# Kernel tuning notes

Measured on AMD Instinct MI355X. Metric: run time of the kernel, lower is better.

Reference implementation:

```python
import jax, jax.numpy as jnp
import numpy as np

T = 48  # top-T from init

def setup_inputs() -> dict:
    key = jax.random.key(0)
    ks = jax.random.split(key, 8)
    B, C, H, W = 16, 512, 32, 32
    tc = C // 8
    return {
        "x": jax.random.normal(ks[0], (B, C, H, W), jnp.float32),
        "fW": jax.random.normal(ks[1], (tc, C), jnp.float32) * 0.05,
        "fb": jax.random.normal(ks[2], (tc,), jnp.float32) * 0.05,
        "gW": jax.random.normal(ks[3], (tc, C), jnp.float32) * 0.05,
        "gb": jax.random.normal(ks[4], (tc,), jnp.float32) * 0.05,
        "hW": jax.random.normal(ks[5], (C, C), jnp.float32) * 0.05,
        "hb": jax.random.normal(ks[6], (C,), jnp.float32) * 0.05,
        "scale": jax.random.normal(ks[7], (1,), jnp.float32),
    }

def reference(x, fW, fb, gW, gb, hW, hb, scale):
    B, C, H, W = x.shape
    tc = fW.shape[0]
    HW = H * W
    # normalize by Frobenius norm over (batch, channel) -> [H, W]
    xn = x / jnp.linalg.norm(x, axis=(0, 1))[None, None]  # [B,C,H,W]
    # 1x1 convs, output already channel-last [B,H,W,out]
    f = jnp.einsum('bchw,oc->bhwo', xn, fW) + fb          # [B,H,W,tc]
    g = jnp.einsum('bchw,oc->bhwo', xn, gW) + gb          # [B,H,W,tc]
    h = jnp.einsum('bchw,oc->bhwo', xn, hW) + hb          # [B,H,W,C]
    xp = jnp.transpose(xn, (0, 2, 3, 1))                  # [B,H,W,C]
    # scores: queries H-major, keys W-major (faithful to permute(0,3,2,1).reshape)
    g_keys = jnp.transpose(g, (0, 3, 2, 1)).reshape(B, tc, HW)  # [B,tc,W*H]
    s = jnp.matmul(f.reshape(B, HW, tc), g_keys)          # [B,HW,HW]
    beta = jax.nn.softmax(s, axis=-1)
    o = jnp.matmul(beta, h.reshape(B, HW, C)).reshape(B, H, W, C)
    fdd = scale * o + xp                                  # [B,H,W,C]
    # per-batch correlation: fdd[b] ([H,W,C]) @ fdd[b].reshape(C,HW)
    corr = jnp.einsum('bhwc,bcn->bhwn', fdd, fdd.reshape(B, C, HW))  # [B,H,W,HW]
    top = jax.lax.top_k(corr, T)[0]                       # descending top-T values
    top = jax.nn.relu(top)
    top = top / jnp.linalg.norm(top, axis=(0, 1))[None, None]  # norm over (B,H) -> [W,T]
    return jnp.transpose(top, (0, 3, 1, 2))               # [B,T,H,W]
```

## Files before the change

kernel.cpp:

```cpp
#include <hip/hip_runtime.h>
#include <cstdint>
#include <cstddef>

#define B_   16
#define C_   512
#define H_   32
#define W_   32
#define HW_  1024
#define TC_  64
#define T_   48

typedef unsigned short u16;
typedef __attribute__((ext_vector_type(8))) short short8v;
typedef __attribute__((ext_vector_type(4))) float f32x4;

__device__ __forceinline__ u16 tobf(float x) {
    unsigned u = __float_as_uint(x);
    return (u16)((u + 0x7FFFu + ((u >> 16) & 1u)) >> 16);
}
__device__ __forceinline__ float frombf(u16 h) {
    return __uint_as_float(((unsigned)h) << 16);
}

__device__ __forceinline__ void gld16(const void* g, void* l) {
    __builtin_amdgcn_global_load_lds(
        (const __attribute__((address_space(1))) void*)g,
        (__attribute__((address_space(3))) void*)l, 16, 0, 0);
}

__global__ void k_colsq(const float* __restrict__ x, float* __restrict__ partial) {
    int bid = blockIdx.x;
    int col = (bid & 3) * 256 + threadIdx.x;
    int r0  = (bid >> 2) * 256;
    const float* p = x + (size_t)r0 * HW_ + col;
    float s = 0.f;
    for (int r = 0; r < 256; ++r) { float v = p[(size_t)r * HW_]; s += v * v; }
    partial[(size_t)(bid >> 2) * HW_ + col] = s;
}

__global__ void k_rsqrt(const float* __restrict__ partial, float* __restrict__ ninv) {
    int i = blockIdx.x * 256 + threadIdx.x;
    if (i < HW_) {
        float s = 0.f;
        for (int r = 0; r < 32; ++r) s += partial[(size_t)r * HW_ + i];
        ninv[i] = rsqrtf(s);
    }
}

__global__ void k_transpose(const float* __restrict__ x, const float* __restrict__ ninv,
                            u16* __restrict__ obH) {
    __shared__ float tile[32][33];
    int b  = blockIdx.z;
    int m0 = blockIdx.x * 32, c0 = blockIdx.y * 32;
    int tx = threadIdx.x, ty = threadIdx.y;
    const float* xb = x + (size_t)b * C_ * HW_;
    #pragma unroll
    for (int j = 0; j < 32; j += 8)
        tile[ty + j][tx] = xb[(size_t)(c0 + ty + j) * HW_ + m0 + tx];
    __syncthreads();
    size_t base = (size_t)b * HW_ * C_;
    #pragma unroll
    for (int j = 0; j < 32; j += 8) {
        int m = m0 + ty + j;
        obH[base + (size_t)m * C_ + c0 + tx] = tobf(tile[tx][ty + j] * ninv[m]);
    }
}

__global__ void k_packW(const float* __restrict__ in, u16* __restrict__ oh) {
    size_t i = (size_t)blockIdx.x * 256 + threadIdx.x;
    oh[i] = tobf(in[i]);
}
__global__ void k_packFG(const float* __restrict__ fW, const float* __restrict__ gW,
                         const float* __restrict__ fb, const float* __restrict__ gb,
                         u16* __restrict__ oh, float* __restrict__ fgb) {
    int idx = blockIdx.x * 256 + threadIdx.x;
    int row = idx >> 9, c = idx & 511;
    float v = (row < 64) ? fW[row * 512 + c] : gW[(row - 64) * 512 + c];
    oh[idx] = tobf(v);
    if (idx < 128) fgb[idx] = (idx < 64) ? fb[idx] : gb[idx - 64];
}

template<int PERMB, int EPI>
__global__ __launch_bounds__(256) void k_gemm1(
    const u16* __restrict__ A, const u16* __restrict__ Bm,
    const float* __restrict__ bias,
    float* __restrict__ Cf, u16* __restrict__ Ch,
    const float* __restrict__ scaleP,
    int N, int K, int lda, int ldb, long sA, long sB, long sC)
{
    __shared__ u16 lds[2 * 8192];
    const int b = blockIdx.z;
    const u16* pA = A + (size_t)b * sA;
    const u16* pB = Bm + (size_t)b * sB;
    const int m0 = blockIdx.y * 128, n0 = blockIdx.x * 128;
    const int tid = threadIdx.x, wave = tid >> 6, lane = tid & 63;
    const int wm = wave >> 1, wn = wave & 1;
    const int g = lane >> 4;

    f32x4 acc[4][4];
    #pragma unroll
    for (int i = 0; i < 4; ++i)
        #pragma unroll
        for (int j = 0; j < 4; ++j) { f32x4 z = {0.f,0.f,0.f,0.f}; acc[i][j] = z; }

    auto STAGE = [&](int kt, int half) {
        const int k0 = kt << 5;
        u16* lb = lds + half * 8192;
        #pragma unroll
        for (int q = 0; q < 4; ++q) {
            int ci = wave * 4 + q;
            bool isA = ci < 8;
            int li = ci & 7;
            const u16* gp = isA ? pA : pB;
            int ld = isA ? lda : ldb;
            int rb = isA ? m0 : n0;
            int rp = li * 8 + (lane >> 3);
            int gg = (lane & 7) ^ (rp & 7);
            int r  = rp * 2 + (gg >> 2);
            int kc = k0 + (gg & 3) * 8;
            int rowg = rb + r;
            if (PERMB && !isA) rowg = ((rowg & 31) << 5) | (rowg >> 5);
            gld16(gp + (size_t)rowg * ld + kc,
                  lb + (isA ? 0 : 4096) + li * 512 + lane * 8);
        }
    };
    auto COMPUTE = [&](int half) {
        const u16* As = lds + half * 8192;
        const u16* Bs = As + 4096;
        short8v av[4];
        #pragma unroll
        for (int i = 0; i < 4; ++i) {
            int r = wm * 64 + i * 16 + (lane & 15);
            int rp = r >> 1, gg = ((r & 1) << 2) + g;
            av[i] = *(const short8v*)(As + rp * 64 + ((gg ^ (rp & 7)) << 3));
        }
        #pragma unroll
        for (int j = 0; j < 4; ++j) {
            int r = wn * 64 + j * 16 + (lane & 15);
            int rp = r >> 1, gg = ((r & 1) << 2) + g;
            short8v bv = *(const short8v*)(Bs + rp * 64 + ((gg ^ (rp & 7)) << 3));
            #pragma unroll
            for (int i = 0; i < 4; ++i)
                acc[i][j] = __builtin_amdgcn_mfma_f32_16x16x32_bf16(av[i], bv, acc[i][j], 0, 0, 0);
        }
    };

    const int nkt = K >> 5;
    STAGE(0, 0);
    int cur = 0;
    for (int kt = 0; kt < nkt; ++kt) {
        if (kt + 1 < nkt) {
            STAGE(kt + 1, cur ^ 1);
            asm volatile("s_waitcnt vmcnt(4)" ::: "memory");
        } else {
            asm volatile("s_waitcnt vmcnt(0)" ::: "memory");
        }
        __builtin_amdgcn_s_barrier();
        __builtin_amdgcn_sched_barrier(0);
        COMPUTE(cur);
        __builtin_amdgcn_sched_barrier(0);
        __builtin_amdgcn_s_barrier();
        cur ^= 1;
    }

    const float sc = (EPI == 2) ? scaleP[0] : 0.f;
    const int colbase = n0 + wn * 64 + (lane & 15);
    const int rowbase = m0 + wm * 64 + ((lane >> 4) << 2);
    #pragma unroll
    for (int i = 0; i < 4; ++i)
        #pragma unroll
        for (int j = 0; j < 4; ++j) {
            int col = colbase + j * 16;
            #pragma unroll
            for (int rg = 0; rg < 4; ++rg) {
                int row = rowbase + i * 16 + rg;
                size_t idx = (size_t)b * sC + (size_t)row * N + col;
                float a = acc[i][j][rg];
                if (EPI == 0)      Cf[idx] = a;
                else if (EPI == 2) Ch[idx] = tobf(sc * a + frombf(Ch[idx]));
                else if (EPI == 4) Ch[idx] = tobf(a);
                else if (EPI == 5) Ch[idx] = tobf(a + bias[row]);
                else               Ch[idx] = tobf(a + bias[col]);
            }
        }
}

template<int PERMB, int EPI>
__global__ __launch_bounds__(512) void k_gemm2(
    const u16* __restrict__ A, const u16* __restrict__ Bm,
    const float* __restrict__ bias,
    float* __restrict__ Cf, u16* __restrict__ Ch,
    const float* __restrict__ scaleP,
    int N, int K, int lda, int ldb, long sA, long sB, long sC)
{
    __shared__ u16 lds[2 * 12288];
    const int b = blockIdx.z;
    const u16* pA = A + (size_t)b * sA;
    const u16* pB = Bm + (size_t)b * sB;
    const int m0 = blockIdx.y * 128, n0 = blockIdx.x * 256;
    const int tid = threadIdx.x, wave = tid >> 6, lane = tid & 63;
    const int wm = wave >> 2, wn = wave & 3;
    const int g = lane >> 4;

    f32x4 acc[4][4];
    #pragma unroll
    for (int i = 0; i < 4; ++i)
        #pragma unroll
        for (int j = 0; j < 4; ++j) { f32x4 z = {0.f,0.f,0.f,0.f}; acc[i][j] = z; }

    auto STAGE = [&](int kt, int half) {
        const int k0 = kt << 5;
        u16* lb = lds + half * 12288;
        #pragma unroll
        for (int q = 0; q < 3; ++q) {
            int ci = wave * 3 + q;
            bool isA = ci < 8;
            int li = isA ? ci : ci - 8;
            const u16* gp = isA ? pA : pB;
            int ld = isA ? lda : ldb;
            int rb = isA ? m0 : n0;
            int rp = li * 8 + (lane >> 3);
            int gg = (lane & 7) ^ (rp & 7);
            int r  = rp * 2 + (gg >> 2);
            int kc = k0 + (gg & 3) * 8;
            int rowg = rb + r;
            if (PERMB && !isA) rowg = ((rowg & 31) << 5) | (rowg >> 5);
            gld16(gp + (size_t)rowg * ld + kc,
                  lb + (isA ? 0 : 4096) + li * 512 + lane * 8);
        }
    };
    auto COMPUTE = [&](int half) {
        const u16* As = lds + half * 12288;
        const u16* Bs = As + 4096;
        short8v av[4];
        #pragma unroll
        for (int i = 0; i < 4; ++i) {
            int r = wm * 64 + i * 16 + (lane & 15);
            int rp = r >> 1, gg = ((r & 1) << 2) + g;
            av[i] = *(const short8v*)(As + rp * 64 + ((gg ^ (rp & 7)) << 3));
        }
        #pragma unroll
        for (int j = 0; j < 4; ++j) {
            int r = wn * 64 + j * 16 + (lane & 15);
            int rp = r >> 1, gg = ((r & 1) << 2) + g;
            short8v bv = *(const short8v*)(Bs + rp * 64 + ((gg ^ (rp & 7)) << 3));
            #pragma unroll
            for (int i = 0; i < 4; ++i)
                acc[i][j] = __builtin_amdgcn_mfma_f32_16x16x32_bf16(av[i], bv, acc[i][j], 0, 0, 0);
        }
    };

    const int nkt = K >> 5;
    STAGE(0, 0);
    int cur = 0;
    for (int kt = 0; kt < nkt; ++kt) {
        if (kt + 1 < nkt) {
            STAGE(kt + 1, cur ^ 1);
            asm volatile("s_waitcnt vmcnt(3)" ::: "memory");
        } else {
            asm volatile("s_waitcnt vmcnt(0)" ::: "memory");
        }
        __builtin_amdgcn_s_barrier();
        __builtin_amdgcn_sched_barrier(0);
        COMPUTE(cur);
        __builtin_amdgcn_sched_barrier(0);
        __builtin_amdgcn_s_barrier();
        cur ^= 1;
    }

    const float sc = (EPI == 2) ? scaleP[0] : 0.f;
    const int colbase = n0 + wn * 64 + (lane & 15);
    const int rowbase = m0 + wm * 64 + ((lane >> 4) << 2);
    #pragma unroll
    for (int i = 0; i < 4; ++i)
        #pragma unroll
        for (int j = 0; j < 4; ++j) {
            int col = colbase + j * 16;
            #pragma unroll
            for (int rg = 0; rg < 4; ++rg) {
                int row = rowbase + i * 16 + rg;
                size_t idx = (size_t)b * sC + (size_t)row * N + col;
                float a = acc[i][j][rg];
                if (EPI == 0)      Cf[idx] = a;
                else if (EPI == 2) Ch[idx] = tobf(sc * a + frombf(Ch[idx]));
                else if (EPI == 4) Ch[idx] = tobf(a);
                else if (EPI == 5) Ch[idx] = tobf(a + bias[row]);
                else               Ch[idx] = tobf(a + bias[col]);
            }
        }
}

__global__ __launch_bounds__(256) void k_softmax(u16* __restrict__ S) {
    size_t row = blockIdx.x;
    u16* r = S + row * (size_t)HW_;
    int t = threadIdx.x;
    ushort4 raw = ((const ushort4*)r)[t];
    float v0 = frombf(raw.x), v1 = frombf(raw.y), v2 = frombf(raw.z), v3 = frombf(raw.w);

    __shared__ float redm[4], reds[4];
    int wid = t >> 6, lane = t & 63;

    float m = fmaxf(fmaxf(v0, v1), fmaxf(v2, v3));
    for (int o = 32; o > 0; o >>= 1) m = fmaxf(m, __shfl_down(m, o));
    if (lane == 0) redm[wid] = m;
    __syncthreads();
    if (t == 0) redm[0] = fmaxf(fmaxf(redm[0], redm[1]), fmaxf(redm[2], redm[3]));
    __syncthreads();
    m = redm[0];

    v0 = expf(v0 - m); v1 = expf(v1 - m); v2 = expf(v2 - m); v3 = expf(v3 - m);
    float s = v0 + v1 + v2 + v3;
    for (int o = 32; o > 0; o >>= 1) s += __shfl_down(s, o);
    if (lane == 0) reds[wid] = s;
    __syncthreads();
    if (t == 0) reds[0] = reds[0] + reds[1] + reds[2] + reds[3];
    __syncthreads();
    float inv = 1.f / reds[0];
    ushort4 o4;
    o4.x = tobf(v0 * inv); o4.y = tobf(v1 * inv);
    o4.z = tobf(v2 * inv); o4.w = tobf(v3 * inv);
    ((ushort4*)r)[t] = o4;
}

__global__ void k_tposeU1(const u16* __restrict__ src, u16* __restrict__ dst) {
    __shared__ u16 tile[32][33];
    int b = blockIdx.z;
    const u16* sb = src + (size_t)b * (C_ * HW_);
    u16* db = dst + (size_t)b * (C_ * HW_);
    int c0 = blockIdx.x * 32, r0 = blockIdx.y * 32;
    int tx = threadIdx.x, ty = threadIdx.y;
    #pragma unroll
    for (int j = 0; j < 32; j += 8)
        tile[ty + j][tx] = sb[(size_t)(r0 + ty + j) * HW_ + c0 + tx];
    __syncthreads();
    #pragma unroll
    for (int j = 0; j < 32; j += 8)
        db[(size_t)(c0 + ty + j) * C_ + r0 + tx] = tile[tx][ty + j];
}

__device__ __forceinline__ float sort64_desc(float v, int lane) {
    #pragma unroll
    for (int k = 2; k <= 64; k <<= 1) {
        #pragma unroll
        for (int j = k >> 1; j > 0; j >>= 1) {
            float o = __shfl_xor(v, j);
            bool takeMax = (((lane & k) == 0) == ((lane & j) == 0));
            v = takeMax ? fmaxf(v, o) : fminf(v, o);
        }
    }
    return v;
}
__device__ __forceinline__ float bmerge64_desc(float a, float b, int lane) {
    float br = __shfl(b, 63 - lane);
    float c = fmaxf(a, br);
    #pragma unroll
    for (int j = 32; j > 0; j >>= 1) {
        float o = __shfl_xor(c, j);
        c = ((lane & j) == 0) ? fmaxf(c, o) : fminf(c, o);
    }
    return c;
}

__global__ __launch_bounds__(256) void k_topk(const float* __restrict__ corr,
                                              float* __restrict__ topv) {
    __shared__ float buf[4][1024];
    int wave = threadIdx.x >> 6, lane = threadIdx.x & 63;
    int row = blockIdx.x * 4 + wave;
    const float4* rp = (const float4*)(corr + (size_t)row * HW_);

    float4 e[4];
    #pragma unroll
    for (int q = 0; q < 4; ++q) e[q] = rp[lane * 4 + q];

    float gm = -INFINITY;
    #pragma unroll
    for (int q = 0; q < 4; ++q)
        gm = fmaxf(gm, fmaxf(fmaxf(e[q].x, e[q].y), fmaxf(e[q].z, e[q].w)));
    float sorted = sort64_desc(gm, lane);
    float tau = __shfl(sorted, T_ - 1);

    int c = 0;
    #pragma unroll
    for (int q = 0; q < 4; ++q)
        c += (e[q].x >= tau) + (e[q].y >= tau) + (e[q].z >= tau) + (e[q].w >= tau);
    int sc = c;
    #pragma unroll
    for (int o = 1; o < 64; o <<= 1) {
        int t2 = __shfl_up(sc, o);
        if (lane >= o) sc += t2;
    }
    int off = sc - c;
    int cnt = __shfl(sc, 63);

    float* wb = buf[wave];
    #pragma unroll
    for (int q = 0; q < 4; ++q) {
        if (e[q].x >= tau) wb[off++] = e[q].x;
        if (e[q].y >= tau) wb[off++] = e[q].y;
        if (e[q].z >= tau) wb[off++] = e[q].z;
        if (e[q].w >= tau) wb[off++] = e[q].w;
    }

    float* orow = topv + (size_t)row * T_;
    if (cnt <= 64) {
        float a = (lane < cnt) ? wb[lane] : -INFINITY;
        a = sort64_desc(a, lane);
        if (lane < T_) orow[lane] = fmaxf(a, 0.f);
    } else if (cnt <= 128) {
        float a  = sort64_desc(wb[lane], lane);
        float b2 = sort64_desc((lane < cnt - 64) ? wb[64 + lane] : -INFINITY, lane);
        float m2 = bmerge64_desc(a, b2, lane);
        if (lane < T_) orow[lane] = fmaxf(m2, 0.f);
    } else {
        int P = 256; while (P < cnt) P <<= 1;
        for (int i = cnt + lane; i < P; i += 64) wb[i] = -INFINITY;
        for (int k = 2; k <= P; k <<= 1)
            for (int j = k >> 1; j > 0; j >>= 1)
                for (int t2 = lane; t2 < P; t2 += 64) {
                    int ixj = t2 ^ j;
                    if (ixj > t2) {
                        float a = wb[t2], b3 = wb[ixj];
                        bool desc = ((t2 & k) == 0);
                        if (desc ? (a < b3) : (a > b3)) { wb[t2] = b3; wb[ixj] = a; }
                    }
                }
        if (lane < T_) orow[lane] = fmaxf(wb[lane], 0.f);
    }
}

__global__ void k_colss(const float* __restrict__ topv, float* __restrict__ colss) {
    int o = blockIdx.x;
    int w = o / T_, t = o % T_;
    int lane = threadIdx.x;
    float s = 0.f;
    for (int i = lane; i < 512; i += 64) {
        int b = i >> 5, h = i & 31;
        float v = topv[(size_t)((b << 10) + (h << 5) + w) * T_ + t];
        s += v * v;
    }
    for (int off = 32; off > 0; off >>= 1) s += __shfl_down(s, off);
    if (lane == 0) colss[o] = s;
}

__global__ void k_final(const float* __restrict__ topv, const float* __restrict__ colss,
                        float* __restrict__ out) {
    int idx = blockIdx.x * 256 + threadIdx.x;
    if (idx >= B_ * T_ * HW_) return;
    int w = idx & 31;
    int h = (idx >> 5) & 31;
    int t = (idx >> 10) % T_;
    int b = idx / (T_ * HW_);
    float v = topv[(size_t)((b << 10) + (h << 5) + w) * T_ + t];
    out[idx] = v * rsqrtf(colss[w * T_ + t]);
}

extern "C" void kernel_launch(void* const* d_in, const int* in_sizes, int n_in,
                              void* d_out, int out_size, void* d_ws, size_t ws_size,
                              hipStream_t stream) {
    const float* x     = (const float*)d_in[0];
    const float* fW    = (const float*)d_in[1];
    const float* fb    = (const float*)d_in[2];
    const float* gW    = (const float*)d_in[3];
    const float* gb    = (const float*)d_in[4];
    const float* hW    = (const float*)d_in[5];
    const float* hb    = (const float*)d_in[6];
    const float* scale = (const float*)d_in[7];
    float* out = (float*)d_out;

    char* wsb = (char*)d_ws;
    float* part = (float*)(wsb + 0);
    float* ninv = (float*)(wsb + 131072);
    u16*   hWh  = (u16*)(wsb + 135168);
    u16*   fgWh = (u16*)(wsb + 1183744);
    float* fgb  = (float*)(wsb + 1445888);
    u16*   xnH  = (u16*)(wsb + 1446400);
    u16*   fgH  = (u16*)(wsb + 35000832);
    u16*   fgL  = (u16*)(wsb + 39195136);
    u16*   hvTH = (u16*)(wsb + 43389440);
    float* S    = (float*)(wsb + 76943872);
    float* topv = (float*)fgH;
    float* colss= (float*)fgL;
    u16*   Sp   = (u16*)S;

    const long sXn = 524288;
    const long sFG = 131072;
    const long sS  = 1048576;

    k_colsq<<<128, 256, 0, stream>>>(x, part);
    k_rsqrt<<<4, 256, 0, stream>>>(part, ninv);

    k_transpose<<<dim3(32, 16, 16), dim3(32, 8), 0, stream>>>(x, ninv, xnH);

    k_packW<<<1024, 256, 0, stream>>>(hW, hWh);
    k_packFG<<<256, 256, 0, stream>>>(fW, gW, fb, gb, fgWh, fgb);

    k_gemm1<0, 6><<<dim3(1, 8, 16), 256, 0, stream>>>(
        xnH, fgWh, fgb, nullptr, fgH, nullptr,
        128, 512, 512, 512, sXn, 0, sFG);

    k_gemm2<0, 5><<<dim3(4, 4, 16), 512, 0, stream>>>(
        hWh, xnH, hb, nullptr, hvTH, nullptr,
        1024, 512, 512, 512, 0, sXn, sXn);

    k_gemm2<1, 4><<<dim3(4, 8, 16), 512, 0, stream>>>(
        fgH, fgH + 64, nullptr, nullptr, Sp, nullptr,
        1024, 64, 128, 128, sFG, sFG, sS);

    k_softmax<<<B_ * HW_, 256, 0, stream>>>(Sp);

    k_gemm2<0, 2><<<dim3(2, 8, 16), 512, 0, stream>>>(
        Sp, hvTH, nullptr, nullptr, xnH, scale,
        512, 1024, 1024, 1024, sS, sXn, sXn);

    k_tposeU1<<<dim3(32, 16, 16), dim3(32, 8), 0, stream>>>(xnH, hvTH);

    k_gemm2<0, 0><<<dim3(4, 8, 16), 512, 0, stream>>>(
        xnH, hvTH, nullptr, S, nullptr, nullptr,
        1024, 512, 512, 512, sXn, sXn, sS);

    k_topk<<<B_ * HW_ / 4, 256, 0, stream>>>(S, topv);

    k_colss<<<W_ * T_, 64, 0, stream>>>(topv, colss);
    k_final<<<(B_ * T_ * HW_ + 255) / 256, 256, 0, stream>>>(topv, colss, out);
}
```

Before: 213.8 us.

## Fuse correlation GEMM with top-k selection and retile other GEMMs

Replaces the separate correlation GEMM and top-k kernels with one fused kernel. Each block computes a 32x1024 strip of the correlation matrix with bf16 MFMA, double-buffers its LDS loads, then selects the top-48 per row straight from LDS. This removes the write and re-read of the 64 MB fp32 score matrix. It also doubles the column-norm partial blocks and moves two GEMMs to the smaller-tile gemm1 variant with more blocks, and shrinks the workspace offsets to match. The fused kernel uses about 132 KB of LDS, which limits occupancy to one block per CU. Its grid is only 512 blocks.

```diff
diff --git a/kernel.cpp b/kernel.cpp
--- a/kernel.cpp
+++ b/kernel.cpp
@@ -31,10 +31,10 @@
 __global__ void k_colsq(const float* __restrict__ x, float* __restrict__ partial) {
     int bid = blockIdx.x;
     int col = (bid & 3) * 256 + threadIdx.x;
-    int r0  = (bid >> 2) * 256;
+    int r0  = (bid >> 2) * 128;
     const float* p = x + (size_t)r0 * HW_ + col;
     float s = 0.f;
-    for (int r = 0; r < 256; ++r) { float v = p[(size_t)r * HW_]; s += v * v; }
+    for (int r = 0; r < 128; ++r) { float v = p[(size_t)r * HW_]; s += v * v; }
     partial[(size_t)(bid >> 2) * HW_ + col] = s;
 }
 
@@ -42,7 +42,7 @@
     int i = blockIdx.x * 256 + threadIdx.x;
     if (i < HW_) {
         float s = 0.f;
-        for (int r = 0; r < 32; ++r) s += partial[(size_t)r * HW_ + i];
+        for (int r = 0; r < 64; ++r) s += partial[(size_t)r * HW_ + i];
         ninv[i] = rsqrtf(s);
     }
 }
@@ -361,70 +361,147 @@
     return c;
 }
 
-__global__ __launch_bounds__(256) void k_topk(const float* __restrict__ corr,
-                                              float* __restrict__ topv) {
-    __shared__ float buf[4][1024];
-    int wave = threadIdx.x >> 6, lane = threadIdx.x & 63;
-    int row = blockIdx.x * 4 + wave;
-    const float4* rp = (const float4*)(corr + (size_t)row * HW_);
-
-    float4 e[4];
-    #pragma unroll
-    for (int q = 0; q < 4; ++q) e[q] = rp[lane * 4 + q];
-
-    float gm = -INFINITY;
-    #pragma unroll
-    for (int q = 0; q < 4; ++q)
-        gm = fmaxf(gm, fmaxf(fmaxf(e[q].x, e[q].y), fmaxf(e[q].z, e[q].w)));
-    float sorted = sort64_desc(gm, lane);
-    float tau = __shfl(sorted, T_ - 1);
-
-    int c = 0;
-    #pragma unroll
-    for (int q = 0; q < 4; ++q)
-        c += (e[q].x >= tau) + (e[q].y >= tau) + (e[q].z >= tau) + (e[q].w >= tau);
-    int sc = c;
-    #pragma unroll
-    for (int o = 1; o < 64; o <<= 1) {
-        int t2 = __shfl_up(sc, o);
-        if (lane >= o) sc += t2;
-    }
-    int off = sc - c;
-    int cnt = __shfl(sc, 63);
-
-    float* wb = buf[wave];
-    #pragma unroll
-    for (int q = 0; q < 4; ++q) {
-        if (e[q].x >= tau) wb[off++] = e[q].x;
-        if (e[q].y >= tau) wb[off++] = e[q].y;
-        if (e[q].z >= tau) wb[off++] = e[q].z;
-        if (e[q].w >= tau) wb[off++] = e[q].w;
-    }
-
-    float* orow = topv + (size_t)row * T_;
-    if (cnt <= 64) {
-        float a = (lane < cnt) ? wb[lane] : -INFINITY;
-        a = sort64_desc(a, lane);
-        if (lane < T_) orow[lane] = fmaxf(a, 0.f);
-    } else if (cnt <= 128) {
-        float a  = sort64_desc(wb[lane], lane);
-        float b2 = sort64_desc((lane < cnt - 64) ? wb[64 + lane] : -INFINITY, lane);
-        float m2 = bmerge64_desc(a, b2, lane);
-        if (lane < T_) orow[lane] = fmaxf(m2, 0.f);
-    } else {
-        int P = 256; while (P < cnt) P <<= 1;
-        for (int i = cnt + lane; i < P; i += 64) wb[i] = -INFINITY;
-        for (int k = 2; k <= P; k <<= 1)
-            for (int j = k >> 1; j > 0; j >>= 1)
-                for (int t2 = lane; t2 < P; t2 += 64) {
-                    int ixj = t2 ^ j;
-                    if (ixj > t2) {
-                        float a = wb[t2], b3 = wb[ixj];
-                        bool desc = ((t2 & k) == 0);
-                        if (desc ? (a < b3) : (a > b3)) { wb[t2] = b3; wb[ixj] = a; }
-                    }
-                }
-        if (lane < T_) orow[lane] = fmaxf(wb[lane], 0.f);
+__global__ __launch_bounds__(512) void k_corrtopk(
+    const u16* __restrict__ A,
+    const u16* __restrict__ Bm,
+    float* __restrict__ topv)
+{
+    __shared__ u16 lds[67584];
+    const int b = blockIdx.y;
+    const int m0 = blockIdx.x * 32;
+    const u16* pA = A + (size_t)b * 524288;
+    const u16* pB = Bm + (size_t)b * 524288;
+    const int tid = threadIdx.x, wave = tid >> 6, lane = tid & 63;
+    const int g = lane >> 4;
+
+    f32x4 acc[2][8];
+    #pragma unroll
+    for (int i = 0; i < 2; ++i)
+        #pragma unroll
+        for (int j = 0; j < 8; ++j) { f32x4 z = {0.f,0.f,0.f,0.f}; acc[i][j] = z; }
+
+    auto STAGE = [&](int kt, int half) {
+        const int k0 = kt << 5;
+        u16* lb = lds + half * 33792;
+        #pragma unroll
+        for (int q = 0; q < 8; ++q) {
+            int li = wave * 8 + q;
+            int rp = li * 8 + (lane >> 3);
+            int gg = (lane & 7) ^ (rp & 7);
+            int r  = rp * 2 + (gg >> 2);
+            int kc = k0 + (gg & 3) * 8;
+            gld16(pB + (size_t)r * 512 + kc, lb + li * 512 + lane * 8);
+        }
+        if (lane < 16) {
+            int rp = wave * 2 + (lane >> 3);
+            int gg = (lane & 7) ^ (rp & 7);
+            int r  = rp * 2 + (gg >> 2);
+            int kc = k0 + (gg & 3) * 8;
+            gld16(pA + (size_t)(m0 + r) * 512 + kc,
+                  lb + 32768 + wave * 128 + lane * 8);
+        }
+    };
+    auto COMPUTE = [&](int half) {
+        const u16* Bs = lds + half * 33792;
+        const u16* As = Bs + 32768;
+        short8v av[2];
+        #pragma unroll
+        for (int i = 0; i < 2; ++i) {
+            int r = i * 16 + (lane & 15);
+            int rp = r >> 1, gg = ((r & 1) << 2) + g;
+            av[i] = *(const short8v*)(As + rp * 64 + ((gg ^ (rp & 7)) << 3));
+        }
+        #pragma unroll
+        for (int j = 0; j < 8; ++j) {
+            int n = wave * 128 + j * 16 + (lane & 15);
+            int rp = n >> 1, gg = ((n & 1) << 2) + g;
+            short8v bv = *(const short8v*)(Bs + rp * 64 + ((gg ^ (rp & 7)) << 3));
+            #pragma unroll
+            for (int i = 0; i < 2; ++i)
+                acc[i][j] = __builtin_amdgcn_mfma_f32_16x16x32_bf16(av[i], bv, acc[i][j], 0, 0, 0);
+        }
+    };
+
+    STAGE(0, 0);
+    int cur = 0;
+    for (int kt = 0; kt < 16; ++kt) {
+        if (kt + 1 < 16) {
+            STAGE(kt + 1, cur ^ 1);
+            asm volatile("s_waitcnt vmcnt(9)" ::: "memory");
+        } else {
+            asm volatile("s_waitcnt vmcnt(0)" ::: "memory");
+        }
+        __builtin_amdgcn_s_barrier();
+        __builtin_amdgcn_sched_barrier(0);
+        COMPUTE(cur);
+        __builtin_amdgcn_sched_barrier(0);
+        __builtin_amdgcn_s_barrier();
+        cur ^= 1;
+    }
+
+    __syncthreads();
+    float* rows = (float*)lds;
+    #pragma unroll
+    for (int i = 0; i < 2; ++i) {
+        int rb = i * 16 + ((lane >> 4) << 2);
+        #pragma unroll
+        for (int j = 0; j < 8; ++j) {
+            int col = wave * 128 + j * 16 + (lane & 15);
+            #pragma unroll
+            for (int rg = 0; rg < 4; ++rg)
+                rows[(rb + rg) * 1024 + col] = acc[i][j][rg];
+        }
+    }
+    __syncthreads();
+
+    float* wb = rows + 32768 + wave * 128;
+    for (int ro = 0; ro < 4; ++ro) {
+        int lrow = wave * 4 + ro;
+        const float* rd = rows + (size_t)lrow * 1024;
+        float e[16];
+        #pragma unroll
+        for (int q = 0; q < 16; ++q) e[q] = rd[q * 64 + lane];
+
+        float gm = e[0];
+        #pragma unroll
+        for (int q = 1; q < 16; ++q) gm = fmaxf(gm, e[q]);
+        float sorted = sort64_desc(gm, lane);
+        float tau = __shfl(sorted, T_ - 1);
+
+        int c = 0;
+        #pragma unroll
+        for (int q = 0; q < 16; ++q) c += (e[q] >= tau);
+        int sc2 = c;
+        #pragma unroll
+        for (int o = 1; o < 64; o <<= 1) {
+            int t2 = __shfl_up(sc2, o);
+            if (lane >= o) sc2 += t2;
+        }
+        int off = sc2 - c;
+        int cnt = __shfl(sc2, 63);
+
+        float* orow = topv + ((size_t)b * HW_ + m0 + lrow) * T_;
+        if (cnt <= 128) {
+            #pragma unroll
+            for (int q = 0; q < 16; ++q)
+                if (e[q] >= tau) wb[off++] = e[q];
+            if (cnt <= 64) {
+                float a = (lane < cnt) ? wb[lane] : -INFINITY;
+                a = sort64_desc(a, lane);
+                if (lane < T_) orow[lane] = fmaxf(a, 0.f);
+            } else {
+                float a  = sort64_desc(wb[lane], lane);
+                float b2 = sort64_desc((lane < cnt - 64) ? wb[64 + lane] : -INFINITY, lane);
+                float m2 = bmerge64_desc(a, b2, lane);
+                if (lane < T_) orow[lane] = fmaxf(m2, 0.f);
+            }
+        } else {
+            float m = sort64_desc(e[0], lane);
+            #pragma unroll
+            for (int q = 1; q < 16; ++q)
+                m = bmerge64_desc(m, sort64_desc(e[q], lane), lane);
+            if (lane < T_) orow[lane] = fmaxf(m, 0.f);
+        }
     }
 }
 
@@ -469,15 +546,15 @@
 
     char* wsb = (char*)d_ws;
     float* part = (float*)(wsb + 0);
-    float* ninv = (float*)(wsb + 131072);
-    u16*   hWh  = (u16*)(wsb + 135168);
-    u16*   fgWh = (u16*)(wsb + 1183744);
-    float* fgb  = (float*)(wsb + 1445888);
-    u16*   xnH  = (u16*)(wsb + 1446400);
-    u16*   fgH  = (u16*)(wsb + 35000832);
-    u16*   fgL  = (u16*)(wsb + 39195136);
-    u16*   hvTH = (u16*)(wsb + 43389440);
-    float* S    = (float*)(wsb + 76943872);
+    float* ninv = (float*)(wsb + 262144);
+    u16*   hWh  = (u16*)(wsb + 266240);
+    u16*   fgWh = (u16*)(wsb + 790528);
+    float* fgb  = (float*)(wsb + 921600);
+    u16*   xnH  = (u16*)(wsb + 922112);
+    u16*   fgH  = (u16*)(wsb + 17699328);
+    u16*   fgL  = (u16*)(wsb + 21893632);
+    u16*   hvTH = (u16*)(wsb + 26087936);
+    float* S    = (float*)(wsb + 42865152);
     float* topv = (float*)fgH;
     float* colss= (float*)fgL;
     u16*   Sp   = (u16*)S;
@@ -486,7 +563,7 @@
     const long sFG = 131072;
     const long sS  = 1048576;
 
-    k_colsq<<<128, 256, 0, stream>>>(x, part);
+    k_colsq<<<256, 256, 0, stream>>>(x, part);
     k_rsqrt<<<4, 256, 0, stream>>>(part, ninv);
 
     k_transpose<<<dim3(32, 16, 16), dim3(32, 8), 0, stream>>>(x, ninv, xnH);
@@ -498,7 +575,7 @@
         xnH, fgWh, fgb, nullptr, fgH, nullptr,
         128, 512, 512, 512, sXn, 0, sFG);
 
-    k_gemm2<0, 5><<<dim3(4, 4, 16), 512, 0, stream>>>(
+    k_gemm1<0, 5><<<dim3(8, 4, 16), 256, 0, stream>>>(
         hWh, xnH, hb, nullptr, hvTH, nullptr,
         1024, 512, 512, 512, 0, sXn, sXn);
 
@@ -508,17 +585,13 @@
 
     k_softmax<<<B_ * HW_, 256, 0, stream>>>(Sp);
 
-    k_gemm2<0, 2><<<dim3(2, 8, 16), 512, 0, stream>>>(
+    k_gemm1<0, 2><<<dim3(4, 8, 16), 256, 0, stream>>>(
         Sp, hvTH, nullptr, nullptr, xnH, scale,
         512, 1024, 1024, 1024, sS, sXn, sXn);
 
     k_tposeU1<<<dim3(32, 16, 16), dim3(32, 8), 0, stream>>>(xnH, hvTH);
 
-    k_gemm2<0, 0><<<dim3(4, 8, 16), 512, 0, stream>>>(
-        xnH, hvTH, nullptr, S, nullptr, nullptr,
-        1024, 512, 512, 512, sXn, sXn, sS);
-
-    k_topk<<<B_ * HW_ / 4, 256, 0, stream>>>(S, topv);
+    k_corrtopk<<<dim3(32, 16), 512, 0, stream>>>(xnH, hvTH, topv);
 
     k_colss<<<W_ * T_, 64, 0, stream>>>(topv, colss);
     k_final<<<(B_ * T_ * HW_ + 255) / 256, 256, 0, stream>>>(topv, colss, out);
```

Measured after the change: 222.9 us. +4.3%, slower.
